# Kernel optimization log

Measured on AMD Instinct MI355X. Metric: run time of the kernel, lower is better.

Reference implementation:

```python
import jax, jax.numpy as jnp
import numpy as np

D_MODEL = 1024
NUM_HEADS = 16
DEPTH = D_MODEL // NUM_HEADS


def setup_inputs() -> dict:
    key = jax.random.key(0)
    ks = jax.random.split(key, 11)
    B, S = 2, 2048
    s = 1.0 / np.sqrt(D_MODEL)
    return {
        "q": jax.random.normal(ks[0], (B, S, D_MODEL), jnp.float32),
        "k": jax.random.normal(ks[1], (B, S, D_MODEL), jnp.float32),
        "v": jax.random.normal(ks[2], (B, S, D_MODEL), jnp.float32),
        "wq": jax.random.normal(ks[3], (D_MODEL, D_MODEL), jnp.float32) * s,
        "bq": jax.random.normal(ks[4], (D_MODEL,), jnp.float32) * s,
        "wk": jax.random.normal(ks[5], (D_MODEL, D_MODEL), jnp.float32) * s,
        "bk": jax.random.normal(ks[6], (D_MODEL,), jnp.float32) * s,
        "wv": jax.random.normal(ks[7], (D_MODEL, D_MODEL), jnp.float32) * s,
        "bv": jax.random.normal(ks[8], (D_MODEL,), jnp.float32) * s,
        "wo": jax.random.normal(ks[9], (D_MODEL, D_MODEL), jnp.float32) * s,
        "bo": jax.random.normal(ks[10], (D_MODEL,), jnp.float32) * s,
    }


def _split_heads(x, B):
    # [B, S, D] -> [B, H, S, depth]
    return x.reshape(B, -1, NUM_HEADS, DEPTH).transpose(0, 2, 1, 3)


def reference(q, k, v, wq, bq, wk, bk, wv, bv, wo, bo):
    B, S, _ = q.shape
    # torch Linear: y = x @ W.T + b
    qh = _split_heads(q @ wq.T + bq, B)
    kh = _split_heads(k @ wk.T + bk, B)
    vh = _split_heads(v @ wv.T + bv, B)
    scale = jnp.sqrt(jnp.asarray(DEPTH, jnp.float32))
    scores = jnp.einsum("bhqd,bhkd->bhqk", qh, kh) / scale  # [B,H,S,S]
    attn = jax.nn.softmax(scores, axis=-1)
    out = jnp.einsum("bhqk,bhkd->bhqd", attn, vh)
    out = out.transpose(0, 2, 1, 3).reshape(B, S, D_MODEL)
    return out @ wo.T + bo
```

## Files before the change

### kernel.cpp

```cpp
#include <hip/hip_runtime.h>
#include <hip/hip_bf16.h>
#include <math.h>

#define D_MODEL 1024
#define NUM_HEADS 16
#define DEPTH 64
#define BATCH 2
#define SEQ 2048
#define N_TOK (BATCH * SEQ)

typedef short bf16x8 __attribute__((ext_vector_type(8)));
typedef _Float16 f16x8 __attribute__((ext_vector_type(8)));
typedef float f32x4  __attribute__((ext_vector_type(4)));
typedef unsigned short u16x8 __attribute__((ext_vector_type(8)));
typedef unsigned short u16x4 __attribute__((ext_vector_type(4)));

__device__ __forceinline__ unsigned short f2b(float x) {
    return __builtin_bit_cast(unsigned short, __float2bfloat16(x));
}
__device__ __forceinline__ float b2f(unsigned short h) {
    return __builtin_bit_cast(float, (unsigned int)h << 16);
}
__device__ __forceinline__ unsigned short f2h(float x) {
    return __builtin_bit_cast(unsigned short, (_Float16)x);
}

__global__ __launch_bounds__(256) void split_f16(
    const float* __restrict__ src,
    unsigned short* __restrict__ dst,
    int n8)
{
    const int i = blockIdx.x * 256 + threadIdx.x;
    if (i >= n8) return;
    const float4 f0 = ((const float4*)src)[2 * i];
    const float4 f1 = ((const float4*)src)[2 * i + 1];
    const float xs[8] = {f0.x, f0.y, f0.z, f0.w, f1.x, f1.y, f1.z, f1.w};
    u16x8 o;
    #pragma unroll
    for (int e = 0; e < 8; ++e) o[e] = f2h(xs[e]);
    *(u16x8*)&dst[(size_t)i * 8] = o;
}

__global__ __launch_bounds__(256) void prep_weights(
    const float* __restrict__ s0, const float* __restrict__ s1,
    const float* __restrict__ s2, const float* __restrict__ s3,
    unsigned short* __restrict__ f0, unsigned short* __restrict__ f1,
    unsigned short* __restrict__ f2,
    unsigned short* __restrict__ h3, unsigned short* __restrict__ l3,
    int n8)
{
    const int i = blockIdx.x * 256 + threadIdx.x;
    if (i >= n8) return;
    const int which = blockIdx.y;
    const float* src = (which == 0) ? s0 : (which == 1) ? s1 : (which == 2) ? s2 : s3;
    const float4 a0 = ((const float4*)src)[2 * i];
    const float4 a1 = ((const float4*)src)[2 * i + 1];
    const float xs[8] = {a0.x, a0.y, a0.z, a0.w, a1.x, a1.y, a1.z, a1.w};
    if (which < 3) {
        unsigned short* dst = (which == 0) ? f0 : (which == 1) ? f1 : f2;
        u16x8 o;
        #pragma unroll
        for (int e = 0; e < 8; ++e) o[e] = f2h(xs[e]);
        *(u16x8*)&dst[(size_t)i * 8] = o;
    } else {
        u16x8 h8, l8;
        #pragma unroll
        for (int e = 0; e < 8; ++e) {
            const unsigned short h = f2b(xs[e]);
            h8[e] = h;
            l8[e] = f2b(xs[e] - b2f(h));
        }
        *(u16x8*)&h3[(size_t)i * 8] = h8;
        *(u16x8*)&l3[(size_t)i * 8] = l8;
    }
}

__global__ __launch_bounds__(256, 4) void gemm_f16(
    const unsigned short* __restrict__ Af,
    const unsigned short* __restrict__ Bf,
    const float* __restrict__ bias,
    void* __restrict__ Yv,
    float scale,
    int mode)
{
    __shared__ unsigned short sA[2][64][64];
    __shared__ unsigned short sB[2][64][64];

    const int tid  = threadIdx.x;
    const int wave = tid >> 6;
    const int lane = tid & 63;
    const int quad = lane >> 4;
    const int l16  = lane & 15;
    const int wm   = wave >> 1;
    const int wn   = wave & 1;

    const int j0 = blockIdx.x * 64;
    const int i0 = blockIdx.y * 64;

    const int sc  = tid & 7;
    const int r32 = tid >> 3;

    f32x4 acc[2][2] = {};

    auto stage = [&](int buf, int s) {
        const int k0 = s * 64;
        #pragma unroll
        for (int p = 0; p < 4; ++p) {
            const bool isA = p < 2;
            const int row = (p & 1) * 32 + r32;
            const unsigned short* src = isA ? Af : Bf;
            const int grow = (isA ? i0 : j0) + row;
            const int cg = (sc ^ (row & 7)) * 8;
            unsigned short (*dst)[64] = isA ? sA[buf] : sB[buf];
            __builtin_amdgcn_global_load_lds(
                (const __attribute__((address_space(1))) unsigned int*)
                    &src[(size_t)grow * 1024 + k0 + cg],
                (__attribute__((address_space(3))) unsigned int*)&dst[row][sc * 8],
                16, 0, 0);
        }
    };

    stage(0, 0);
    __asm__ volatile("s_waitcnt vmcnt(0)" ::: "memory");
    __syncthreads();

    int cur = 0;
    for (int s = 0; s < 16; ++s) {
        if (s + 1 < 16) stage(cur ^ 1, s + 1);

        #pragma unroll
        for (int ks = 0; ks < 2; ++ks) {
            f16x8 a[2], b[2];
            #pragma unroll
            for (int mt = 0; mt < 2; ++mt) {
                const int row = wm * 32 + mt * 16 + l16;
                const int c = (((ks * 4 + quad) ^ (row & 7))) * 8;
                a[mt] = *(const f16x8*)&sA[cur][row][c];
            }
            #pragma unroll
            for (int nt = 0; nt < 2; ++nt) {
                const int row = wn * 32 + nt * 16 + l16;
                const int c = (((ks * 4 + quad) ^ (row & 7))) * 8;
                b[nt] = *(const f16x8*)&sB[cur][row][c];
            }
            #pragma unroll
            for (int mt = 0; mt < 2; ++mt)
                #pragma unroll
                for (int nt = 0; nt < 2; ++nt)
                    acc[mt][nt] = __builtin_amdgcn_mfma_f32_16x16x32_f16(a[mt], b[nt], acc[mt][nt], 0, 0, 0);
        }

        __asm__ volatile("s_waitcnt vmcnt(0)" ::: "memory");
        __syncthreads();
        cur ^= 1;
    }

    float bv[2];
    #pragma unroll
    for (int nt = 0; nt < 2; ++nt)
        bv[nt] = bias[j0 + wn * 32 + nt * 16 + l16];

    #pragma unroll
    for (int mt = 0; mt < 2; ++mt) {
        const int ibase = i0 + wm * 32 + mt * 16 + quad * 4;
        #pragma unroll
        for (int nt = 0; nt < 2; ++nt) {
            const int j = j0 + wn * 32 + nt * 16 + l16;
            const int h = j >> 6, d = j & 63;
            if (mode == 1) {
                __hip_bfloat16* Y = (__hip_bfloat16*)Yv;
                #pragma unroll
                for (int r = 0; r < 4; ++r) {
                    const int i = ibase + r;
                    const int b = i >> 11, ss = i & (SEQ - 1);
                    Y[(((size_t)(b * NUM_HEADS + h) * SEQ) + ss) * DEPTH + d] =
                        __float2bfloat16((acc[mt][nt][r] + bv[nt]) * scale);
                }
            } else {
                unsigned short* Y = (unsigned short*)Yv;
                const int b = ibase >> 11;
                u16x4 pack;
                #pragma unroll
                for (int r = 0; r < 4; ++r)
                    pack[r] = f2b((acc[mt][nt][r] + bv[nt]) * scale);
                *(u16x4*)&Y[(((size_t)(b * NUM_HEADS + h) * DEPTH) + d) * SEQ
                            + (ibase & (SEQ - 1))] = pack;
            }
        }
    }
}

__global__ __launch_bounds__(512, 2) void gemm_bf16x3(
    const unsigned short* __restrict__ Ahi,
    const unsigned short* __restrict__ Alo,
    const unsigned short* __restrict__ Bhi,
    const unsigned short* __restrict__ Blo,
    const float* __restrict__ bias,
    float* __restrict__ Y,
    float scale)
{
    __shared__ unsigned short sAh[128][64];
    __shared__ unsigned short sAl[128][64];
    __shared__ unsigned short sBh[128][64];
    __shared__ unsigned short sBl[128][64];

    const int tid  = threadIdx.x;
    const int wave = tid >> 6;
    const int lane = tid & 63;
    const int quad = lane >> 4;
    const int l16  = lane & 15;
    const int wm   = wave >> 1;
    const int wn   = wave & 1;

    const int j0 = blockIdx.x * 128;
    const int i0 = blockIdx.y * 128;

    const int sc  = tid & 7;
    const int r64 = tid >> 3;

    u16x8 preH[4], preL[4];

    #pragma unroll
    for (int p = 0; p < 4; ++p) {
        const int row256 = p * 64 + r64;
        const bool isA = row256 < 128;
        const int row = isA ? row256 : row256 - 128;
        const unsigned short* srcH = isA ? Ahi : Bhi;
        const unsigned short* srcL = isA ? Alo : Blo;
        const int grow = (isA ? i0 : j0) + row;
        const int cg = (sc ^ (row & 7)) * 8;
        const size_t go = (size_t)grow * 1024 + cg;
        preH[p] = *(const u16x8*)&srcH[go];
        preL[p] = *(const u16x8*)&srcL[go];
    }

    f32x4 acc[2][4] = {};

    for (int s = 0; s < 16; ++s) {
        __syncthreads();

        #pragma unroll
        for (int p = 0; p < 4; ++p) {
            const int row256 = p * 64 + r64;
            const bool isA = row256 < 128;
            const int row = isA ? row256 : row256 - 128;
            unsigned short (*dh)[64] = isA ? sAh : sBh;
            unsigned short (*dl)[64] = isA ? sAl : sBl;
            *(u16x8*)&dh[row][sc * 8] = preH[p];
            *(u16x8*)&dl[row][sc * 8] = preL[p];
        }
        __syncthreads();

        if (s + 1 < 16) {
            const int k0 = (s + 1) * 64;
            #pragma unroll
            for (int p = 0; p < 4; ++p) {
                const int row256 = p * 64 + r64;
                const bool isA = row256 < 128;
                const int row = isA ? row256 : row256 - 128;
                const unsigned short* srcH = isA ? Ahi : Bhi;
                const unsigned short* srcL = isA ? Alo : Blo;
                const int grow = (isA ? i0 : j0) + row;
                const int cg = (sc ^ (row & 7)) * 8;
                const size_t go = (size_t)grow * 1024 + k0 + cg;
                preH[p] = *(const u16x8*)&srcH[go];
                preL[p] = *(const u16x8*)&srcL[go];
            }
        }

        #pragma unroll
        for (int ks = 0; ks < 2; ++ks) {
            bf16x8 ah[2], al[2], bh[4], bl[4];
            #pragma unroll
            for (int mt = 0; mt < 2; ++mt) {
                const int row = wm * 32 + mt * 16 + l16;
                const int c = (((ks * 4 + quad) ^ (row & 7))) * 8;
                ah[mt] = *(const bf16x8*)&sAh[row][c];
                al[mt] = *(const bf16x8*)&sAl[row][c];
            }
            #pragma unroll
            for (int nt = 0; nt < 4; ++nt) {
                const int row = wn * 64 + nt * 16 + l16;
                const int c = (((ks * 4 + quad) ^ (row & 7))) * 8;
                bh[nt] = *(const bf16x8*)&sBh[row][c];
                bl[nt] = *(const bf16x8*)&sBl[row][c];
            }
            #pragma unroll
            for (int mt = 0; mt < 2; ++mt)
                #pragma unroll
                for (int nt = 0; nt < 4; ++nt) {
                    acc[mt][nt] = __builtin_amdgcn_mfma_f32_16x16x32_bf16(ah[mt], bh[nt], acc[mt][nt], 0, 0, 0);
                    acc[mt][nt] = __builtin_amdgcn_mfma_f32_16x16x32_bf16(ah[mt], bl[nt], acc[mt][nt], 0, 0, 0);
                    acc[mt][nt] = __builtin_amdgcn_mfma_f32_16x16x32_bf16(al[mt], bh[nt], acc[mt][nt], 0, 0, 0);
                }
        }
    }

    float bv[4];
    #pragma unroll
    for (int nt = 0; nt < 4; ++nt)
        bv[nt] = bias[j0 + wn * 64 + nt * 16 + l16];

    #pragma unroll
    for (int mt = 0; mt < 2; ++mt) {
        const int ibase = i0 + wm * 32 + mt * 16 + quad * 4;
        #pragma unroll
        for (int nt = 0; nt < 4; ++nt) {
            const int j = j0 + wn * 64 + nt * 16 + l16;
            #pragma unroll
            for (int r = 0; r < 4; ++r)
                Y[(size_t)(ibase + r) * 1024 + j] = (acc[mt][nt][r] + bv[nt]) * scale;
        }
    }
}

__global__ __launch_bounds__(256) void flash_attn_mfma(
    const __hip_bfloat16* __restrict__ Qg,
    const __hip_bfloat16* __restrict__ Kg,
    const __hip_bfloat16* __restrict__ Vg,
    unsigned short* __restrict__ OHi,
    unsigned short* __restrict__ OLo)
{
    __shared__ unsigned short Ks[64][72];
    __shared__ unsigned short Vt[64][72];
    __shared__ unsigned short Ps[4][16][68];

    const int tid  = threadIdx.x;
    const int wave = tid >> 6;
    const int lane = tid & 63;
    const int quad = lane >> 4;
    const int l16  = lane & 15;

    const int bh = blockIdx.x >> 5;
    const int q0 = (blockIdx.x & 31) * 64;

    const unsigned short* Qu = (const unsigned short*)Qg + (size_t)bh * SEQ * DEPTH;
    const unsigned short* Ku = (const unsigned short*)Kg + (size_t)bh * SEQ * DEPTH;
    const unsigned short* Vu = (const unsigned short*)Vg + (size_t)bh * DEPTH * SEQ;

    const int qrow = q0 + wave * 16 + l16;
    bf16x8 qf[2];
    qf[0] = *(const bf16x8*)&Qu[(size_t)qrow * DEPTH + quad * 8];
    qf[1] = *(const bf16x8*)&Qu[(size_t)qrow * DEPTH + 32 + quad * 8];

    bf16x8 ones;
    #pragma unroll
    for (int e = 0; e < 8; ++e) ones[e] = (short)0x3F80;

    f32x4 o_acc[4] = {};
    f32x4 l_acc = {0.f, 0.f, 0.f, 0.f};

    const int srow = tid >> 3;
    const int sc8  = (tid & 7) * 8;
    u16x8 kpre[2], vpre[2];
    #pragma unroll
    for (int it = 0; it < 2; ++it) {
        const int row = it * 32 + srow;
        kpre[it] = *(const u16x8*)&Ku[(size_t)row * DEPTH + sc8];
        vpre[it] = *(const u16x8*)&Vu[(size_t)row * SEQ + sc8];
    }

    for (int t = 0; t < 32; ++t) {
        __syncthreads();

        #pragma unroll
        for (int it = 0; it < 2; ++it) {
            const int row = it * 32 + srow;
            *(u16x8*)&Ks[row][sc8] = kpre[it];
            *(u16x8*)&Vt[row][sc8] = vpre[it];
        }
        __syncthreads();

        if (t + 1 < 32) {
            const int k0 = (t + 1) * 64;
            #pragma unroll
            for (int it = 0; it < 2; ++it) {
                const int row = it * 32 + srow;
                kpre[it] = *(const u16x8*)&Ku[(size_t)(k0 + row) * DEPTH + sc8];
                vpre[it] = *(const u16x8*)&Vu[(size_t)row * SEQ + k0 + sc8];
            }
        }

        f32x4 s[4];
        #pragma unroll
        for (int nt = 0; nt < 4; ++nt) {
            s[nt] = f32x4{0.f, 0.f, 0.f, 0.f};
            bf16x8 kf0 = *(const bf16x8*)&Ks[nt * 16 + l16][quad * 8];
            s[nt] = __builtin_amdgcn_mfma_f32_16x16x32_bf16(qf[0], kf0, s[nt], 0, 0, 0);
            bf16x8 kf1 = *(const bf16x8*)&Ks[nt * 16 + l16][32 + quad * 8];
            s[nt] = __builtin_amdgcn_mfma_f32_16x16x32_bf16(qf[1], kf1, s[nt], 0, 0, 0);
        }

        #pragma unroll
        for (int nt = 0; nt < 4; ++nt)
            #pragma unroll
            for (int r = 0; r < 4; ++r)
                Ps[wave][quad * 4 + r][nt * 16 + l16] = f2b(__expf(s[nt][r]));

        __builtin_amdgcn_wave_barrier();
        __asm__ volatile("s_waitcnt lgkmcnt(0)" ::: "memory");
        __builtin_amdgcn_wave_barrier();

        bf16x8 pf[2];
        {
            u16x4 a0 = *(const u16x4*)&Ps[wave][l16][quad * 8];
            u16x4 a1 = *(const u16x4*)&Ps[wave][l16][quad * 8 + 4];
            u16x4 b0 = *(const u16x4*)&Ps[wave][l16][32 + quad * 8];
            u16x4 b1 = *(const u16x4*)&Ps[wave][l16][32 + quad * 8 + 4];
            #pragma unroll
            for (int e = 0; e < 4; ++e) {
                pf[0][e] = (short)a0[e]; pf[0][4 + e] = (short)a1[e];
                pf[1][e] = (short)b0[e]; pf[1][4 + e] = (short)b1[e];
            }
        }

        #pragma unroll
        for (int nt = 0; nt < 4; ++nt) {
            bf16x8 vf0 = *(const bf16x8*)&Vt[nt * 16 + l16][quad * 8];
            o_acc[nt] = __builtin_amdgcn_mfma_f32_16x16x32_bf16(pf[0], vf0, o_acc[nt], 0, 0, 0);
            bf16x8 vf1 = *(const bf16x8*)&Vt[nt * 16 + l16][32 + quad * 8];
            o_acc[nt] = __builtin_amdgcn_mfma_f32_16x16x32_bf16(pf[1], vf1, o_acc[nt], 0, 0, 0);
        }
        l_acc = __builtin_amdgcn_mfma_f32_16x16x32_bf16(pf[0], ones, l_acc, 0, 0, 0);
        l_acc = __builtin_amdgcn_mfma_f32_16x16x32_bf16(pf[1], ones, l_acc, 0, 0, 0);
    }

    const int b = bh / NUM_HEADS;
    const int h = bh % NUM_HEADS;
    #pragma unroll
    for (int r = 0; r < 4; ++r) {
        const float inv = 1.f / l_acc[r];
        const int row = q0 + wave * 16 + quad * 4 + r;
        #pragma unroll
        for (int nt = 0; nt < 4; ++nt) {
            const float o = o_acc[nt][r] * inv;
            const size_t idx = ((size_t)(b * SEQ + row)) * D_MODEL + h * DEPTH + nt * 16 + l16;
            const unsigned short hbits = f2b(o);
            OHi[idx] = hbits;
            OLo[idx] = f2b(o - b2f(hbits));
        }
    }
}

extern "C" void kernel_launch(void* const* d_in, const int* in_sizes, int n_in,
                              void* d_out, int out_size, void* d_ws, size_t ws_size,
                              hipStream_t stream) {
    const float* q  = (const float*)d_in[0];
    const float* k  = (const float*)d_in[1];
    const float* v  = (const float*)d_in[2];
    const float* wq = (const float*)d_in[3];
    const float* bq = (const float*)d_in[4];
    const float* wk = (const float*)d_in[5];
    const float* bk = (const float*)d_in[6];
    const float* wv = (const float*)d_in[7];
    const float* bv = (const float*)d_in[8];
    const float* wo = (const float*)d_in[9];
    const float* bo = (const float*)d_in[10];
    float* out = (float*)d_out;

    char* ws = (char*)d_ws;
    const size_t MB = 1024 * 1024;
    unsigned short* Af16 = (unsigned short*)(ws);
    unsigned short* AoHi = (unsigned short*)(ws);
    unsigned short* AoLo = (unsigned short*)(ws + 8 * MB);
    unsigned short* WqF  = (unsigned short*)(ws + 16 * MB);
    unsigned short* WkF  = (unsigned short*)(ws + 18 * MB);
    unsigned short* WvF  = (unsigned short*)(ws + 20 * MB);
    unsigned short* WoH  = (unsigned short*)(ws + 22 * MB);
    unsigned short* WoL  = (unsigned short*)(ws + 24 * MB);
    __hip_bfloat16* Qh   = (__hip_bfloat16*)(ws + 26 * MB);
    __hip_bfloat16* Kh   = (__hip_bfloat16*)(ws + 34 * MB);
    __hip_bfloat16* Vh   = (__hip_bfloat16*)(ws + 42 * MB);

    const int nW8 = D_MODEL * D_MODEL / 8;
    const int nA8 = N_TOK * D_MODEL / 8;
    dim3 sb(256);

    prep_weights<<<dim3(nW8 / 256, 4), sb, 0, stream>>>(
        wq, wk, wv, wo, WqF, WkF, WvF, WoH, WoL, nW8);

    dim3 fblk(256);
    dim3 fgrid(D_MODEL / 64, N_TOK / 64);

    split_f16<<<dim3(nA8 / 256), sb, 0, stream>>>(q, Af16, nA8);
    gemm_f16<<<fgrid, fblk, 0, stream>>>(Af16, WqF, bq, Qh, 0.125f, 1);
    split_f16<<<dim3(nA8 / 256), sb, 0, stream>>>(k, Af16, nA8);
    gemm_f16<<<fgrid, fblk, 0, stream>>>(Af16, WkF, bk, Kh, 1.0f, 1);
    split_f16<<<dim3(nA8 / 256), sb, 0, stream>>>(v, Af16, nA8);
    gemm_f16<<<fgrid, fblk, 0, stream>>>(Af16, WvF, bv, Vh, 1.0f, 2);

    dim3 ablk(256);
    dim3 agrid(BATCH * NUM_HEADS * (SEQ / 64));
    flash_attn_mfma<<<agrid, ablk, 0, stream>>>(Qh, Kh, Vh, AoHi, AoLo);

    dim3 oblk(512);
    dim3 ogrid(D_MODEL / 128, N_TOK / 128);
    gemm_bf16x3<<<ogrid, oblk, 0, stream>>>(AoHi, AoLo, WoH, WoL, bo, out, 1.0f);
}
```

Before: 272.6 us.

## Fuse f16 input conversion into batched QKV GEMM and use permlane for P

Removes the three split_f16 passes by loading fp32 activations into registers in the GEMM, converting them to f16 and writing them to LDS. It also merges the three projection GEMMs into one launch via gridDim.z, which cuts launches and lets the projections run concurrently. In attention, S is computed transposed (K as the A operand) so the exp'd P tile can be rearranged with permlane32/16 swaps instead of a round trip through LDS. The trade-off is more register pressure and synchronous fp32 loads in the GEMM instead of async global_load_lds for A.

```diff
diff --git a/kernel.cpp b/kernel.cpp
--- a/kernel.cpp
+++ b/kernel.cpp
@@ -14,6 +14,7 @@
 typedef float f32x4  __attribute__((ext_vector_type(4)));
 typedef unsigned short u16x8 __attribute__((ext_vector_type(8)));
 typedef unsigned short u16x4 __attribute__((ext_vector_type(4)));
+typedef unsigned int u32x4 __attribute__((ext_vector_type(4)));
 
 __device__ __forceinline__ unsigned short f2b(float x) {
     return __builtin_bit_cast(unsigned short, __float2bfloat16(x));
@@ -25,20 +26,13 @@
     return __builtin_bit_cast(unsigned short, (_Float16)x);
 }
 
-__global__ __launch_bounds__(256) void split_f16(
-    const float* __restrict__ src,
-    unsigned short* __restrict__ dst,
-    int n8)
-{
-    const int i = blockIdx.x * 256 + threadIdx.x;
-    if (i >= n8) return;
-    const float4 f0 = ((const float4*)src)[2 * i];
-    const float4 f1 = ((const float4*)src)[2 * i + 1];
-    const float xs[8] = {f0.x, f0.y, f0.z, f0.w, f1.x, f1.y, f1.z, f1.w};
-    u16x8 o;
-    #pragma unroll
-    for (int e = 0; e < 8; ++e) o[e] = f2h(xs[e]);
-    *(u16x8*)&dst[(size_t)i * 8] = o;
+__device__ __forceinline__ void pl32_swap(unsigned int& x, unsigned int& y) {
+    auto r = __builtin_amdgcn_permlane32_swap(x, y, false, false);
+    x = (unsigned int)r[0]; y = (unsigned int)r[1];
+}
+__device__ __forceinline__ void pl16_swap(unsigned int& x, unsigned int& y) {
+    auto r = __builtin_amdgcn_permlane16_swap(x, y, false, false);
+    x = (unsigned int)r[0]; y = (unsigned int)r[1];
 }
 
 __global__ __launch_bounds__(256) void prep_weights(
@@ -75,16 +69,25 @@
     }
 }
 
-__global__ __launch_bounds__(256, 4) void gemm_f16(
-    const unsigned short* __restrict__ Af,
-    const unsigned short* __restrict__ Bf,
-    const float* __restrict__ bias,
-    void* __restrict__ Yv,
-    float scale,
-    int mode)
+__global__ __launch_bounds__(256, 4) void qkv_gemm(
+    const float* __restrict__ Aq, const float* __restrict__ Ak,
+    const float* __restrict__ Av,
+    const unsigned short* __restrict__ Wq, const unsigned short* __restrict__ Wk,
+    const unsigned short* __restrict__ Wv,
+    const float* __restrict__ bq, const float* __restrict__ bk,
+    const float* __restrict__ bv,
+    void* __restrict__ Yq, void* __restrict__ Yk, void* __restrict__ Yvp)
 {
     __shared__ unsigned short sA[2][64][64];
     __shared__ unsigned short sB[2][64][64];
+
+    const int z = blockIdx.z;
+    const float* Af = (z == 0) ? Aq : (z == 1) ? Ak : Av;
+    const unsigned short* Bf = (z == 0) ? Wq : (z == 1) ? Wk : Wv;
+    const float* bias = (z == 0) ? bq : (z == 1) ? bk : bv;
+    const float scale = (z == 0) ? 0.125f : 1.0f;
+    const int mode = (z == 2) ? 2 : 1;
+    void* Yv = (z == 0) ? Yq : (z == 1) ? Yk : Yvp;
 
     const int tid  = threadIdx.x;
     const int wave = tid >> 6;
@@ -102,31 +105,54 @@
 
     f32x4 acc[2][2] = {};
 
-    auto stage = [&](int buf, int s) {
+    float4 fq[2][2];
+
+    auto loadA = [&](int s) {
         const int k0 = s * 64;
         #pragma unroll
-        for (int p = 0; p < 4; ++p) {
-            const bool isA = p < 2;
-            const int row = (p & 1) * 32 + r32;
-            const unsigned short* src = isA ? Af : Bf;
-            const int grow = (isA ? i0 : j0) + row;
+        for (int p = 0; p < 2; ++p) {
+            const int row = p * 32 + r32;
             const int cg = (sc ^ (row & 7)) * 8;
-            unsigned short (*dst)[64] = isA ? sA[buf] : sB[buf];
+            const float* srcp = &Af[(size_t)(i0 + row) * 1024 + k0 + cg];
+            fq[p][0] = *(const float4*)srcp;
+            fq[p][1] = *(const float4*)(srcp + 4);
+        }
+    };
+    auto writeA = [&](int buf) {
+        #pragma unroll
+        for (int p = 0; p < 2; ++p) {
+            const int row = p * 32 + r32;
+            const float xs[8] = {fq[p][0].x, fq[p][0].y, fq[p][0].z, fq[p][0].w,
+                                 fq[p][1].x, fq[p][1].y, fq[p][1].z, fq[p][1].w};
+            u16x8 o;
+            #pragma unroll
+            for (int e = 0; e < 8; ++e) o[e] = f2h(xs[e]);
+            *(u16x8*)&sA[buf][row][sc * 8] = o;
+        }
+    };
+    auto stageB = [&](int buf, int s) {
+        const int k0 = s * 64;
+        #pragma unroll
+        for (int p = 0; p < 2; ++p) {
+            const int row = p * 32 + r32;
+            const int cg = (sc ^ (row & 7)) * 8;
             __builtin_amdgcn_global_load_lds(
                 (const __attribute__((address_space(1))) unsigned int*)
-                    &src[(size_t)grow * 1024 + k0 + cg],
-                (__attribute__((address_space(3))) unsigned int*)&dst[row][sc * 8],
+                    &Bf[(size_t)(j0 + row) * 1024 + k0 + cg],
+                (__attribute__((address_space(3))) unsigned int*)&sB[buf][row][sc * 8],
                 16, 0, 0);
         }
     };
 
-    stage(0, 0);
+    loadA(0);
+    stageB(0, 0);
     __asm__ volatile("s_waitcnt vmcnt(0)" ::: "memory");
+    writeA(0);
     __syncthreads();
 
     int cur = 0;
     for (int s = 0; s < 16; ++s) {
-        if (s + 1 < 16) stage(cur ^ 1, s + 1);
+        if (s + 1 < 16) { loadA(s + 1); stageB(cur ^ 1, s + 1); }
 
         #pragma unroll
         for (int ks = 0; ks < 2; ++ks) {
@@ -150,15 +176,18 @@
                     acc[mt][nt] = __builtin_amdgcn_mfma_f32_16x16x32_f16(a[mt], b[nt], acc[mt][nt], 0, 0, 0);
         }
 
-        __asm__ volatile("s_waitcnt vmcnt(0)" ::: "memory");
+        if (s + 1 < 16) {
+            __asm__ volatile("s_waitcnt vmcnt(0)" ::: "memory");
+            writeA(cur ^ 1);
+        }
         __syncthreads();
         cur ^= 1;
     }
 
-    float bv[2];
+    float bvv[2];
     #pragma unroll
     for (int nt = 0; nt < 2; ++nt)
-        bv[nt] = bias[j0 + wn * 32 + nt * 16 + l16];
+        bvv[nt] = bias[j0 + wn * 32 + nt * 16 + l16];
 
     #pragma unroll
     for (int mt = 0; mt < 2; ++mt) {
@@ -174,7 +203,7 @@
                     const int i = ibase + r;
                     const int b = i >> 11, ss = i & (SEQ - 1);
                     Y[(((size_t)(b * NUM_HEADS + h) * SEQ) + ss) * DEPTH + d] =
-                        __float2bfloat16((acc[mt][nt][r] + bv[nt]) * scale);
+                        __float2bfloat16((acc[mt][nt][r] + bvv[nt]) * scale);
                 }
             } else {
                 unsigned short* Y = (unsigned short*)Yv;
@@ -182,7 +211,7 @@
                 u16x4 pack;
                 #pragma unroll
                 for (int r = 0; r < 4; ++r)
-                    pack[r] = f2b((acc[mt][nt][r] + bv[nt]) * scale);
+                    pack[r] = f2b((acc[mt][nt][r] + bvv[nt]) * scale);
                 *(u16x4*)&Y[(((size_t)(b * NUM_HEADS + h) * DEPTH) + d) * SEQ
                             + (ibase & (SEQ - 1))] = pack;
             }
@@ -323,7 +352,6 @@
 {
     __shared__ unsigned short Ks[64][72];
     __shared__ unsigned short Vt[64][72];
-    __shared__ unsigned short Ps[4][16][68];
 
     const int tid  = threadIdx.x;
     const int wave = tid >> 6;
@@ -386,32 +414,41 @@
         for (int nt = 0; nt < 4; ++nt) {
             s[nt] = f32x4{0.f, 0.f, 0.f, 0.f};
             bf16x8 kf0 = *(const bf16x8*)&Ks[nt * 16 + l16][quad * 8];
-            s[nt] = __builtin_amdgcn_mfma_f32_16x16x32_bf16(qf[0], kf0, s[nt], 0, 0, 0);
+            s[nt] = __builtin_amdgcn_mfma_f32_16x16x32_bf16(kf0, qf[0], s[nt], 0, 0, 0);
             bf16x8 kf1 = *(const bf16x8*)&Ks[nt * 16 + l16][32 + quad * 8];
-            s[nt] = __builtin_amdgcn_mfma_f32_16x16x32_bf16(qf[1], kf1, s[nt], 0, 0, 0);
-        }
-
-        #pragma unroll
-        for (int nt = 0; nt < 4; ++nt)
-            #pragma unroll
-            for (int r = 0; r < 4; ++r)
-                Ps[wave][quad * 4 + r][nt * 16 + l16] = f2b(__expf(s[nt][r]));
-
-        __builtin_amdgcn_wave_barrier();
-        __asm__ volatile("s_waitcnt lgkmcnt(0)" ::: "memory");
-        __builtin_amdgcn_wave_barrier();
-
+            s[nt] = __builtin_amdgcn_mfma_f32_16x16x32_bf16(kf1, qf[1], s[nt], 0, 0, 0);
+        }
+
+        unsigned int Wp[4][2];
+        #pragma unroll
+        for (int nt = 0; nt < 4; ++nt) {
+            #pragma unroll
+            for (int b = 0; b < 2; ++b) {
+                const unsigned int lo = f2b(__expf(s[nt][2 * b]));
+                const unsigned int hi = f2b(__expf(s[nt][2 * b + 1]));
+                Wp[nt][b] = lo | (hi << 16);
+            }
+        }
+
+        unsigned int pw[8];
+        #pragma unroll
+        for (int b = 0; b < 2; ++b) {
+            unsigned int x = Wp[0][b], y = Wp[1][b];
+            pl32_swap(x, y);
+            pl16_swap(x, y);
+            pw[b] = x; pw[2 + b] = y;
+            x = Wp[2][b]; y = Wp[3][b];
+            pl32_swap(x, y);
+            pl16_swap(x, y);
+            pw[4 + b] = x; pw[6 + b] = y;
+        }
         bf16x8 pf[2];
         {
-            u16x4 a0 = *(const u16x4*)&Ps[wave][l16][quad * 8];
-            u16x4 a1 = *(const u16x4*)&Ps[wave][l16][quad * 8 + 4];
-            u16x4 b0 = *(const u16x4*)&Ps[wave][l16][32 + quad * 8];
-            u16x4 b1 = *(const u16x4*)&Ps[wave][l16][32 + quad * 8 + 4];
-            #pragma unroll
-            for (int e = 0; e < 4; ++e) {
-                pf[0][e] = (short)a0[e]; pf[0][4 + e] = (short)a1[e];
-                pf[1][e] = (short)b0[e]; pf[1][4 + e] = (short)b1[e];
-            }
+            u32x4 t0, t1;
+            #pragma unroll
+            for (int j = 0; j < 4; ++j) { t0[j] = pw[j]; t1[j] = pw[4 + j]; }
+            pf[0] = __builtin_bit_cast(bf16x8, t0);
+            pf[1] = __builtin_bit_cast(bf16x8, t1);
         }
 
         #pragma unroll
@@ -460,7 +497,6 @@
 
     char* ws = (char*)d_ws;
     const size_t MB = 1024 * 1024;
-    unsigned short* Af16 = (unsigned short*)(ws);
     unsigned short* AoHi = (unsigned short*)(ws);
     unsigned short* AoLo = (unsigned short*)(ws + 8 * MB);
     unsigned short* WqF  = (unsigned short*)(ws + 16 * MB);
@@ -473,21 +509,15 @@
     __hip_bfloat16* Vh   = (__hip_bfloat16*)(ws + 42 * MB);
 
     const int nW8 = D_MODEL * D_MODEL / 8;
-    const int nA8 = N_TOK * D_MODEL / 8;
     dim3 sb(256);
 
     prep_weights<<<dim3(nW8 / 256, 4), sb, 0, stream>>>(
         wq, wk, wv, wo, WqF, WkF, WvF, WoH, WoL, nW8);
 
     dim3 fblk(256);
-    dim3 fgrid(D_MODEL / 64, N_TOK / 64);
-
-    split_f16<<<dim3(nA8 / 256), sb, 0, stream>>>(q, Af16, nA8);
-    gemm_f16<<<fgrid, fblk, 0, stream>>>(Af16, WqF, bq, Qh, 0.125f, 1);
-    split_f16<<<dim3(nA8 / 256), sb, 0, stream>>>(k, Af16, nA8);
-    gemm_f16<<<fgrid, fblk, 0, stream>>>(Af16, WkF, bk, Kh, 1.0f, 1);
-    split_f16<<<dim3(nA8 / 256), sb, 0, stream>>>(v, Af16, nA8);
-    gemm_f16<<<fgrid, fblk, 0, stream>>>(Af16, WvF, bv, Vh, 1.0f, 2);
+    dim3 fgrid(D_MODEL / 64, N_TOK / 64, 3);
+    qkv_gemm<<<fgrid, fblk, 0, stream>>>(
+        q, k, v, WqF, WkF, WvF, bq, bk, bv, Qh, Kh, (void*)Vh);
 
     dim3 ablk(256);
     dim3 agrid(BATCH * NUM_HEADS * (SEQ / 64));
```

Result: no change. 272.1 us (-0.2%).
